# Kernel optimization log

Hardware: AMD Instinct MI355X
Metric: run time of the kernel (lower is better)

Reference implementation:

```python
import jax, jax.numpy as jnp
import numpy as np
from jax import lax

D = 768          # embed_dim
H = 12           # n_heads
DEPTH = 2
T = 6            # n_timepoints
PS = 7           # patch_size
IMG = (56, 49, 49)
GRID = (8, 7, 7)
NPATCH = 392     # prod(GRID), must be even for the sinusoidal PE
SEQ = T * NPATCH # 2352 space-time tokens
MLP_H = 3072     # int(768 * 4.0)
B = 2
RRELU_MLP = 0.4        # eval-mode RReLU(0.1, 0.7) slope
RRELU_HEAD = 11.0/48.0 # eval-mode RReLU(1/8, 1/3) slope


def _ln(x, g, b, eps=1e-6):
    m = x.mean(-1, keepdims=True)
    v = ((x - m) ** 2).mean(-1, keepdims=True)
    return (x - m) / jnp.sqrt(v + eps) * g + b


def _pos_enc(t, d):
    pos = np.arange(t, dtype=np.float32)[:, None]
    div = 1.0 / 10000.0 ** (np.arange(0, d, 2, dtype=np.float32) / d)
    pe = np.zeros((t, d), np.float32)
    pe[:, 0::2] = np.sin(pos * div)
    pe[:, 1::2] = np.cos(pos * div)
    return jnp.asarray(pe)


def _convT_dw(x, w, bias, stride, dilation):
    # depthwise ConvTranspose3d(C, C, k, stride, dilation, groups=C); w: (C,1,k,k,k)
    C = x.shape[1]
    k = w.shape[-1]
    wf = jnp.flip(w, axis=(2, 3, 4))
    pad = (k - 1) * dilation
    y = lax.conv_general_dilated(
        x, wf, window_strides=(1, 1, 1), padding=[(pad, pad)] * 3,
        lhs_dilation=(stride,) * 3, rhs_dilation=(dilation,) * 3,
        dimension_numbers=('NCDHW', 'OIDHW', 'NCDHW'), feature_group_count=C)
    return y + bias[None, :, None, None, None]


def _nearest(x, size):
    # torch F.interpolate(mode='nearest'): src = floor(dst * in/out)
    for ax, s in zip((2, 3, 4), size):
        idx = (jnp.arange(s) * (x.shape[ax] / s)).astype(jnp.int32)
        x = jnp.take(x, idx, axis=ax)
    return x


def setup_inputs() -> dict:
    key = jax.random.key(0)
    ks = iter(jax.random.split(key, 64))
    def rn(shape, s=0.02):
        return jax.random.normal(next(ks), shape, jnp.float32) * s
    inp = {}
    inp['x'] = jax.random.normal(next(ks), (B, 1, T) + IMG, jnp.float32)
    inp['pconv_w'] = rn((D, 1, PS, PS, PS)); inp['pconv_b'] = rn((D,))
    inp['pos_embed'] = rn((1, SEQ, D))
    inp['ln1_g'] = jnp.ones((DEPTH, D)); inp['ln1_b'] = jnp.zeros((DEPTH, D))
    inp['qkv_w'] = rn((DEPTH, 3 * D, D)); inp['qkv_b'] = rn((DEPTH, 3 * D))
    inp['proj_w'] = rn((DEPTH, D, D)); inp['proj_b'] = rn((DEPTH, D))
    inp['ln2_g'] = jnp.ones((DEPTH, D)); inp['ln2_b'] = jnp.zeros((DEPTH, D))
    inp['fc1_w'] = rn((DEPTH, MLP_H, D)); inp['fc1_b'] = rn((DEPTH, MLP_H))
    inp['fc2_w'] = rn((DEPTH, D, MLP_H)); inp['fc2_b'] = rn((DEPTH, D))
    inp['normf_g'] = jnp.ones((D,)); inp['normf_b'] = jnp.zeros((D,))
    inp['dfc_w'] = rn((1, D)); inp['dfc_b'] = rn((1,))
    inp['up1_w'] = rn((T, 1, 7, 7, 7)); inp['up1_b'] = rn((T,))
    inp['up2_w'] = rn((T, 1, 5, 5, 5)); inp['up2_b'] = rn((T,))
    inp['up3_w'] = rn((T, 1, 9, 9, 9)); inp['up3_b'] = rn((T,))
    inp['hconv_w'] = rn((T, 1, 1, 1, 1)); inp['hconv_b'] = rn((T,))
    return inp


def reference(x, pconv_w, pconv_b, pos_embed, ln1_g, ln1_b, qkv_w, qkv_b,
              proj_w, proj_b, ln2_g, ln2_b, fc1_w, fc1_b, fc2_w, fc2_b,
              normf_g, normf_b, dfc_w, dfc_b, up1_w, up1_b, up2_w, up2_b,
              up3_w, up3_b, hconv_w, hconv_b):
    b = x.shape[0]
    hd = D // H
    scale = hd ** -0.5
    # fold time into batch, patch-embed each 3D frame
    xt = x.transpose(0, 2, 1, 3, 4, 5).reshape(b * T, 1, *IMG)
    y = lax.conv_general_dilated(
        xt, pconv_w, (PS, PS, PS), 'VALID',
        dimension_numbers=('NCDHW', 'OIDHW', 'NCDHW'))
    y = y + pconv_b[None, :, None, None, None]
    tok = y.reshape(b * T, D, NPATCH).transpose(0, 2, 1).reshape(b, SEQ, D)
    tok = tok + pos_embed
    for i in range(DEPTH):
        h = _ln(tok, ln1_g[i], ln1_b[i])
        qkv = (h @ qkv_w[i].T + qkv_b[i]).reshape(b, SEQ, 3, H, hd)
        qkv = qkv.transpose(2, 0, 3, 1, 4)  # (3,b,H,SEQ,hd)
        q, k, v = qkv[0], qkv[1], qkv[2]
        attn = jax.nn.softmax(jnp.einsum('bhnd,bhmd->bhnm', q, k) * scale, axis=-1)
        o = jnp.einsum('bhnm,bhmd->bhnd', attn, v)
        o = o.transpose(0, 2, 1, 3).reshape(b, SEQ, D)
        tok = tok + (o @ proj_w[i].T + proj_b[i])
        h = _ln(tok, ln2_g[i], ln2_b[i])
        h = h @ fc1_w[i].T + fc1_b[i]
        h = jnp.where(h >= 0, h, RRELU_MLP * h)
        tok = tok + (h @ fc2_w[i].T + fc2_b[i])
    tok = _ln(tok, normf_g, normf_b)
    z = tok.reshape(b, T, NPATCH, D)
    # --- DecoderHead ---
    z = (z @ dfc_w.T + dfc_b)[..., 0]           # (b,T,NPATCH)
    z = z - z.mean(axis=1, keepdims=True)       # subtract time mean
    z = z + _pos_enc(T, NPATCH)
    z = z.reshape(b, T, *GRID)                  # (b,T,8,7,7)
    z = _convT_dw(z, up1_w, up1_b, 1, 1)        # -> (b,T,14,13,13)
    z = _convT_dw(z, up2_w, up2_b, 2, 1)        # -> (b,T,31,29,29)
    z = _convT_dw(z, up3_w, up3_b, 1, 2)        # -> (b,T,47,45,45)
    z = _nearest(z, IMG)                        # -> (b,T,56,49,49)
    z = z * hconv_w[:, 0, 0, 0, 0][None, :, None, None, None] \
        + hconv_b[None, :, None, None, None]
    z = jnp.where(z >= 0, z, RRELU_HEAD * z)
    return z[:, None].transpose(0, 1, 3, 4, 5, 2)  # (b,1,56,49,49,T)
```

## Files before the change

kernel.cpp:

```cpp
#include <hip/hip_runtime.h>


#define AS1 __attribute__((address_space(1)))
#define AS3 __attribute__((address_space(3)))

using bf16 = __bf16;
typedef __bf16 bf16x8 __attribute__((ext_vector_type(8)));
typedef float  f32x4  __attribute__((ext_vector_type(4)));

#define CDIV(a, b) (((a) + (b) - 1) / (b))

__device__ __forceinline__ void gll16(const void* g, void* l) {
  __builtin_amdgcn_global_load_lds((AS1 void*)(void*)g, (AS3 void*)l, 16, 0, 0);
}

template <int SH>
__device__ __forceinline__ float rorf(float x) {
  int i = __builtin_amdgcn_update_dpp(0, __builtin_bit_cast(int, x),
                                      0x120 + SH, 0xF, 0xF, false);
  return __builtin_bit_cast(float, i);
}
__device__ __forceinline__ float rowmax16(float v) {
  v = fmaxf(v, rorf<1>(v)); v = fmaxf(v, rorf<2>(v));
  v = fmaxf(v, rorf<4>(v)); v = fmaxf(v, rorf<8>(v));
  return v;
}
__device__ __forceinline__ float rowsum16(float v) {
  v += rorf<1>(v); v += rorf<2>(v); v += rorf<4>(v); v += rorf<8>(v);
  return v;
}

__global__ __launch_bounds__(256) void gemm_bt(
    const bf16* __restrict__ A, const bf16* __restrict__ B,
    float* Cf, bf16* Cb, const float* __restrict__ bias,
    const float* addp, int addmod, int rrelu,
    int M, int N, int K, int lda, int ldb, int ldc,
    long long sA, long long sB, long long sC, int ksplit) {
  __shared__ __align__(16) bf16 As[128 * 32];
  __shared__ __align__(16) bf16 Bs[128 * 32];
  const int tid  = threadIdx.x;
  const int lane = tid & 63;
  const int wave = tid >> 6;
  const int wm = wave & 1;
  const int wn = wave >> 1;
  const int q  = lane >> 4;
  const int r  = lane & 15;
  const int tm0 = blockIdx.x * 128;
  const int tn0 = blockIdx.y * 128;
  const int z   = blockIdx.z;

  const bf16* Ab = A + (ksplit > 1 ? 0 : (size_t)z * (size_t)sA);
  const bf16* Bb = B + (ksplit > 1 ? 0 : (size_t)z * (size_t)sB);
  const int kc = K / ksplit;
  const int kb = (ksplit > 1) ? z * kc : 0;
  const int ke = (ksplit > 1) ? kb + kc : K;

  const int arow0 = min(tm0 + (tid >> 2), M - 1);
  const int arow1 = min(tm0 + (tid >> 2) + 64, M - 1);
  const int brow0 = min(tn0 + (tid >> 2), N - 1);
  const int brow1 = min(tn0 + (tid >> 2) + 64, N - 1);
  const int kcol  = (tid & 3) * 8;
  const bf16* ap0 = Ab + (size_t)arow0 * lda + kcol;
  const bf16* ap1 = Ab + (size_t)arow1 * lda + kcol;
  const bf16* bp0 = Bb + (size_t)brow0 * ldb + kcol;
  const bf16* bp1 = Bb + (size_t)brow1 * ldb + kcol;
  bf16* asw0 = &As[(wave * 64) * 8];
  bf16* asw1 = &As[(256 + wave * 64) * 8];
  bf16* bsw0 = &Bs[(wave * 64) * 8];
  bf16* bsw1 = &Bs[(256 + wave * 64) * 8];

  f32x4 acc[4][4];
#pragma unroll
  for (int mi = 0; mi < 4; ++mi)
#pragma unroll
    for (int ni = 0; ni < 4; ++ni) acc[mi][ni] = (f32x4){0.f, 0.f, 0.f, 0.f};

  for (int k0 = kb; k0 < ke; k0 += 32) {
    __syncthreads();
    gll16(ap0 + k0, asw0);
    gll16(ap1 + k0, asw1);
    gll16(bp0 + k0, bsw0);
    gll16(bp1 + k0, bsw1);
    __syncthreads();
    bf16x8 af[4], bfr[4];
#pragma unroll
    for (int mi = 0; mi < 4; ++mi)
      af[mi] = *(const bf16x8*)&As[(wm * 64 + mi * 16 + r) * 32 + q * 8];
#pragma unroll
    for (int ni = 0; ni < 4; ++ni)
      bfr[ni] = *(const bf16x8*)&Bs[(wn * 64 + ni * 16 + r) * 32 + q * 8];
#pragma unroll
    for (int mi = 0; mi < 4; ++mi)
#pragma unroll
      for (int ni = 0; ni < 4; ++ni)
        acc[mi][ni] = __builtin_amdgcn_mfma_f32_16x16x32_bf16(
            af[mi], bfr[ni], acc[mi][ni], 0, 0, 0);
  }

  float* cf = Cf ? Cf + (ksplit > 1 ? 0 : (size_t)z * (size_t)sC) : nullptr;
  bf16*  cb = Cb ? Cb + (ksplit > 1 ? 0 : (size_t)z * (size_t)sC) : nullptr;
#pragma unroll
  for (int mi = 0; mi < 4; ++mi) {
    const int row0 = tm0 + wm * 64 + mi * 16 + q * 4;
#pragma unroll
    for (int ni = 0; ni < 4; ++ni) {
      const int col = tn0 + wn * 64 + ni * 16 + r;
      if (col >= N) continue;
      const float bv = bias ? bias[col] : 0.f;
#pragma unroll
      for (int reg = 0; reg < 4; ++reg) {
        const int rr = row0 + reg;
        if (rr >= M) continue;
        if (ksplit > 1) {
          float v = acc[mi][ni][reg] + (z == 0 ? bv : 0.f);
          atomicAdd(&cf[(size_t)rr * ldc + col], v);
        } else {
          float v = acc[mi][ni][reg] + bv;
          if (addp) v += addp[(size_t)(rr % addmod) * ldc + col];
          if (rrelu) v = (v >= 0.f) ? v : 0.4f * v;
          if (cf) cf[(size_t)rr * ldc + col] = v;
          else    cb[(size_t)rr * ldc + col] = (bf16)v;
        }
      }
    }
  }
}

__global__ __launch_bounds__(256) void flash_attn_split(
    const bf16* __restrict__ Qg, const bf16* __restrict__ Kg,
    const bf16* __restrict__ Vt, float* __restrict__ Opart,
    float* __restrict__ Mpart, float* __restrict__ Lpart) {
  __shared__ __align__(16) bf16 Plds[4][2][16 * 72];
  const int lane = threadIdx.x & 63;
  const int wave = threadIdx.x >> 6;
  const int q = lane >> 4, r = lane & 15;
  const int inst = blockIdx.y;
  const int z = blockIdx.z;
  const int rt = blockIdx.x * 4 + wave;
  if (rt >= 74) return;
  const int row0 = rt * 32;
  const int ch0 = (z * 37) >> 1;
  const int ch1 = ((z + 1) * 37) >> 1;
  const bf16* Qi = Qg + (size_t)inst * 2432 * 64;
  const bf16* Ki = Kg + (size_t)inst * 2368 * 64;
  const bf16* Vi = Vt + (size_t)inst * 64 * 2368;

  bf16x8 qf[2][2];
#pragma unroll
  for (int t = 0; t < 2; ++t) {
    qf[t][0] = *(const bf16x8*)&Qi[(size_t)(row0 + t * 16 + r) * 64 + q * 8];
    qf[t][1] = *(const bf16x8*)&Qi[(size_t)(row0 + t * 16 + r) * 64 + 32 + q * 8];
  }

  f32x4 O[2][4];
  float m[2][4], l[2][4];
#pragma unroll
  for (int t = 0; t < 2; ++t)
#pragma unroll
    for (int i = 0; i < 4; ++i) {
      O[t][i] = (f32x4){0.f, 0.f, 0.f, 0.f};
      m[t][i] = -1e30f; l[t][i] = 0.f;
    }

  bf16x8 kf0[4], kf1[4];
#pragma unroll
  for (int ct = 0; ct < 4; ++ct) {
    const bf16* kp = &Ki[(size_t)(ch0 * 64 + ct * 16 + r) * 64 + q * 8];
    kf0[ct] = *(const bf16x8*)kp;
    kf1[ct] = *(const bf16x8*)(kp + 32);
  }

  for (int ch = ch0; ch < ch1; ++ch) {
    const int col0 = ch * 64;
    bf16x8 vf0[4], vf1[4];
#pragma unroll
    for (int ot = 0; ot < 4; ++ot) {
      const bf16* vp = &Vi[(size_t)(ot * 16 + r) * 2368 + col0 + q * 8];
      vf0[ot] = *(const bf16x8*)vp;
      vf1[ot] = *(const bf16x8*)(vp + 32);
    }
    f32x4 s[2][4];
#pragma unroll
    for (int ct = 0; ct < 4; ++ct) {
#pragma unroll
      for (int t = 0; t < 2; ++t) {
        f32x4 a = (f32x4){0.f, 0.f, 0.f, 0.f};
        a = __builtin_amdgcn_mfma_f32_16x16x32_bf16(qf[t][0], kf0[ct], a, 0, 0, 0);
        a = __builtin_amdgcn_mfma_f32_16x16x32_bf16(qf[t][1], kf1[ct], a, 0, 0, 0);
        s[t][ct] = a * 0.125f;
      }
    }
    if (ch == 36) {
      s[0][3] = (f32x4){-1e30f, -1e30f, -1e30f, -1e30f};
      s[1][3] = (f32x4){-1e30f, -1e30f, -1e30f, -1e30f};
    }
    const int chn = (ch + 1 < 37) ? ch + 1 : 36;
#pragma unroll
    for (int ct = 0; ct < 4; ++ct) {
      const bf16* kp = &Ki[(size_t)(chn * 64 + ct * 16 + r) * 64 + q * 8];
      kf0[ct] = *(const bf16x8*)kp;
      kf1[ct] = *(const bf16x8*)(kp + 32);
    }
#pragma unroll
    for (int t = 0; t < 2; ++t) {
      float alpha[4];
#pragma unroll
      for (int reg = 0; reg < 4; ++reg) {
        float v = fmaxf(fmaxf(s[t][0][reg], s[t][1][reg]),
                        fmaxf(s[t][2][reg], s[t][3][reg]));
        v = rowmax16(v);
        float nm = fmaxf(m[t][reg], v);
        alpha[reg] = __expf(m[t][reg] - nm);
        m[t][reg] = nm;
      }
      float csum[4] = {0.f, 0.f, 0.f, 0.f};
#pragma unroll
      for (int ct = 0; ct < 4; ++ct)
#pragma unroll
        for (int reg = 0; reg < 4; ++reg) {
          float p = __expf(s[t][ct][reg] - m[t][reg]);
          s[t][ct][reg] = p;
          csum[reg] += p;
        }
#pragma unroll
      for (int reg = 0; reg < 4; ++reg)
        l[t][reg] = l[t][reg] * alpha[reg] + rowsum16(csum[reg]);
#pragma unroll
      for (int ot = 0; ot < 4; ++ot)
#pragma unroll
        for (int reg = 0; reg < 4; ++reg) O[t][ot][reg] *= alpha[reg];
      bf16* Pw = Plds[wave][t];
#pragma unroll
      for (int ct = 0; ct < 4; ++ct)
#pragma unroll
        for (int reg = 0; reg < 4; ++reg)
          Pw[(q * 4 + reg) * 72 + ct * 16 + r] = (bf16)s[t][ct][reg];
    }
#pragma unroll
    for (int t = 0; t < 2; ++t) {
      const bf16* Pw = Plds[wave][t];
      const bf16x8 pf0 = *(const bf16x8*)&Pw[r * 72 + q * 8];
      const bf16x8 pf1 = *(const bf16x8*)&Pw[r * 72 + 32 + q * 8];
#pragma unroll
      for (int ot = 0; ot < 4; ++ot) {
        O[t][ot] = __builtin_amdgcn_mfma_f32_16x16x32_bf16(pf0, vf0[ot], O[t][ot], 0, 0, 0);
        O[t][ot] = __builtin_amdgcn_mfma_f32_16x16x32_bf16(pf1, vf1[ot], O[t][ot], 0, 0, 0);
      }
    }
  }
#pragma unroll
  for (int t = 0; t < 2; ++t) {
    const int p = (z * 24 + inst) * 152 + rt * 2 + t;
    float* Op = Opart + (size_t)p * 1024;
#pragma unroll
    for (int ot = 0; ot < 4; ++ot)
#pragma unroll
      for (int reg = 0; reg < 4; ++reg)
        Op[(q * 4 + reg) * 64 + ot * 16 + r] = O[t][ot][reg];
    if (r == 0) {
#pragma unroll
      for (int reg = 0; reg < 4; ++reg) {
        Mpart[(size_t)p * 16 + q * 4 + reg] = m[t][reg];
        Lpart[(size_t)p * 16 + q * 4 + reg] = l[t][reg];
      }
    }
  }
}

__global__ __launch_bounds__(256) void attn_combine(
    const float* __restrict__ Opart, const float* __restrict__ Mpart,
    const float* __restrict__ Lpart, bf16* __restrict__ Og) {
  const int tile = blockIdx.x;
  const int inst = blockIdx.y;
  const int bb = inst / 12, hh = inst % 12;
  const int pb = inst * 152 + tile;
#pragma unroll
  for (int i = 0; i < 4; ++i) {
    const int e = threadIdx.x + 256 * i;
    const int row = e >> 6, col = e & 63;
    float mv[2], lv[2];
#pragma unroll
    for (int zz = 0; zz < 2; ++zz) {
      mv[zz] = Mpart[(size_t)(zz * 3648 + pb) * 16 + row];
      lv[zz] = Lpart[(size_t)(zz * 3648 + pb) * 16 + row];
    }
    const float ms = fmaxf(mv[0], mv[1]);
    float lsum = 0.f, osum = 0.f;
#pragma unroll
    for (int zz = 0; zz < 2; ++zz) {
      const float w = __expf(mv[zz] - ms);
      lsum += lv[zz] * w;
      osum += Opart[(size_t)(zz * 3648 + pb) * 1024 + e] * w;
    }
    Og[(size_t)(bb * 2352 + tile * 16 + row) * 768 + hh * 64 + col] =
        (bf16)(osum / lsum);
  }
}


__global__ void cvt_bf16(const float* __restrict__ x, bf16* __restrict__ y, int n) {
  int i = blockIdx.x * 256 + threadIdx.x;
  if (i < n) y[i] = (bf16)x[i];
}

__global__ void prep_pconv(const float* __restrict__ w, bf16* __restrict__ y) {
  int i = blockIdx.x * 256 + threadIdx.x;
  if (i >= 768 * 352) return;
  int d = i / 352, j = i % 352;
  y[i] = (bf16)(j < 343 ? w[d * 343 + j] : 0.f);
}

__global__ void im2col(const float* __restrict__ x, bf16* __restrict__ A) {
  int i = blockIdx.x * 256 + threadIdx.x;
  if (i >= 4704 * 352) return;
  int j = i % 352, tok = i / 352;
  float v = 0.f;
  if (j < 343) {
    int p = tok % 392, bt = tok / 392;
    int kx = j % 7, ky = (j / 7) % 7, kz = j / 49;
    int px = p % 7, py = (p / 7) % 7, pz = p / 49;
    int zz = pz * 7 + kz, yy = py * 7 + ky, xx = px * 7 + kx;
    v = x[(((size_t)bt * 56 + zz) * 49 + yy) * 49 + xx];
  }
  A[i] = (bf16)v;
}

template <typename OT>
__global__ __launch_bounds__(256) void ln_kernel(
    const float* __restrict__ x, const float* __restrict__ g,
    const float* __restrict__ bb, OT* __restrict__ y, int M) {
  int row = blockIdx.x * 4 + (threadIdx.x >> 6);
  int lane = threadIdx.x & 63;
  if (row >= M) return;
  const float* xr = x + (size_t)row * 768;
  float v[12], s = 0.f;
#pragma unroll
  for (int i = 0; i < 12; ++i) { v[i] = xr[lane + i * 64]; s += v[i]; }
#pragma unroll
  for (int off = 32; off; off >>= 1) s += __shfl_xor(s, off, 64);
  float mean = s * (1.f / 768.f);
  float vs = 0.f;
#pragma unroll
  for (int i = 0; i < 12; ++i) { float d = v[i] - mean; vs += d * d; }
#pragma unroll
  for (int off = 32; off; off >>= 1) vs += __shfl_xor(vs, off, 64);
  float inv = 1.f / sqrtf(vs * (1.f / 768.f) + 1e-6f);
#pragma unroll
  for (int i = 0; i < 12; ++i) {
    int j = lane + i * 64;
    y[(size_t)row * 768 + j] = (OT)((v[i] - mean) * inv * g[j] + bb[j]);
  }
}

__global__ __launch_bounds__(256) void repack_qkv(
    const float* __restrict__ qkv, bf16* __restrict__ Q,
    bf16* __restrict__ Kb, bf16* __restrict__ VT) {
  int inst = blockIdx.y;
  int b = inst / 12, h = inst % 12;
  int s = blockIdx.x * 4 + (threadIdx.x >> 6);
  int d = threadIdx.x & 63;
  if (s >= 2432) return;
  size_t qIdx = ((size_t)inst * 2432 + s) * 64 + d;
  if (s >= 2352) {
    Q[qIdx] = (bf16)0.f;
    if (s < 2368) {
      Kb[((size_t)inst * 2368 + s) * 64 + d] = (bf16)0.f;
      VT[((size_t)inst * 64 + d) * 2368 + s] = (bf16)0.f;
    }
    return;
  }
  const float* rowp = qkv + (size_t)(b * 2352 + s) * 2304 + h * 64 + d;
  Q[qIdx] = (bf16)rowp[0];
  Kb[((size_t)inst * 2368 + s) * 64 + d] = (bf16)rowp[768];
  VT[((size_t)inst * 64 + d) * 2368 + s] = (bf16)rowp[1536];
}

__global__ __launch_bounds__(256) void dfc_kernel(
    const float* __restrict__ x, const float* __restrict__ w,
    const float* __restrict__ b0, float* __restrict__ z0, int M) {
  int row = blockIdx.x * 4 + (threadIdx.x >> 6);
  int lane = threadIdx.x & 63;
  if (row >= M) return;
  const float* xr = x + (size_t)row * 768;
  float s = 0.f;
#pragma unroll
  for (int i = 0; i < 12; ++i) s += xr[lane + i * 64] * w[lane + i * 64];
#pragma unroll
  for (int off = 32; off; off >>= 1) s += __shfl_xor(s, off, 64);
  if (lane == 0) z0[row] = s + b0[0];
}

__global__ void head_pe(const float* __restrict__ z0, float* __restrict__ z1) {
  int i = blockIdx.x * 256 + threadIdx.x;
  if (i >= 784) return;
  int b = i / 392, p = i % 392;
  float vals[6], m = 0.f;
#pragma unroll
  for (int t = 0; t < 6; ++t) { vals[t] = z0[(b * 6 + t) * 392 + p]; m += vals[t]; }
  m *= (1.f / 6.f);
  float e = (float)(2 * (p >> 1)) / 392.0f;
  float div = powf(10000.f, -e);
#pragma unroll
  for (int t = 0; t < 6; ++t) {
    float arg = (float)t * div;
    float pe = (p & 1) ? cosf(arg) : sinf(arg);
    z1[(b * 6 + t) * 392 + p] = vals[t] - m + pe;
  }
}

template <int ID, int IH, int IW, int PD, int PH, int PWA, int OFF, int ST>
__global__ void pad_in(const float* __restrict__ x, float* __restrict__ Xp) {
  int i = blockIdx.x * 256 + threadIdx.x;
  constexpr int total = 12 * PD * PH * PWA;
  if (i >= total) return;
  int px = i % PWA, t1 = i / PWA;
  int py = t1 % PH, t2 = t1 / PH;
  int pz = t2 % PD, c = t2 / PD;
  float v = 0.f;
  int tz = pz - OFF, ty = py - OFF, tx = px - OFF;
  if (tz >= 0 && ty >= 0 && tx >= 0 &&
      (ST == 1 || (((tz | ty | tx) & 1) == 0))) {
    int iz = tz / ST, iy = ty / ST, ix = tx / ST;
    if (iz < ID && iy < IH && ix < IW)
      v = x[((size_t)(c * ID + iz) * IH + iy) * IW + ix];
  }
  Xp[i] = v;
}

template <int PD, int PH, int PWA, int OD, int OH, int OW, int K, int DIL>
__global__ __launch_bounds__(256) void convt4(
    const float* __restrict__ Xp, const float* __restrict__ w,
    const float* __restrict__ bias, float* __restrict__ y) {
  constexpr int P0  = (K - 1) * DIL;
  constexpr int QX  = (OW + 3) / 4;
  constexpr int NLD = (P0 + 4 + 3) / 4;
  int idx = blockIdx.x * 256 + threadIdx.x;
  if (idx >= OD * OH * QX) return;
  int c = blockIdx.y;
  int qx = idx % QX; int t1 = idx / QX;
  int oy = t1 % OH;  int oz = t1 / OH;
  int ox0 = qx * 4;
  const float* xc = Xp + (size_t)c * (PD * PH * PWA);
  const float* wc = w + (c % 6) * (K * K * K);
  const float bv = bias[c % 6];
  float a0 = bv, a1 = bv, a2 = bv, a3 = bv;
  for (int kz = 0; kz < K; ++kz) {
    const int bz = oz + P0 - kz * DIL;
#pragma unroll
    for (int ky = 0; ky < K; ++ky) {
      const int by = oy + P0 - ky * DIL;
      const float* base = xc + ((size_t)bz * PH + by) * PWA + ox0;
      float buf[NLD * 4];
#pragma unroll
      for (int i = 0; i < NLD; ++i)
        *(f32x4*)&buf[i * 4] = *(const f32x4*)(base + i * 4);
      const float* wr = wc + (kz * K + ky) * K;
#pragma unroll
      for (int kx = 0; kx < K; ++kx) {
        const float wv = wr[kx];
        const int j = P0 - kx * DIL;
        a0 += wv * buf[j + 0];
        a1 += wv * buf[j + 1];
        a2 += wv * buf[j + 2];
        a3 += wv * buf[j + 3];
      }
    }
  }
  float* yp = y + (size_t)c * (OD * OH * OW) + ((size_t)oz * OH + oy) * OW + ox0;
  yp[0] = a0;
  if (ox0 + 1 < OW) yp[1] = a1;
  if (ox0 + 2 < OW) yp[2] = a2;
  if (ox0 + 3 < OW) yp[3] = a3;
}

__global__ void head_final(const float* __restrict__ z4, const float* __restrict__ hw,
                           const float* __restrict__ hb, float* __restrict__ out) {
  int idx = blockIdx.x * 256 + threadIdx.x;
  if (idx >= 1613472) return;
  int t = idx % 6, rdx = idx / 6;
  int xx = rdx % 49; rdx /= 49;
  int yy = rdx % 49; rdx /= 49;
  int zz = rdx % 56; int b = rdx / 56;
  const float rz = (float)(47.0 / 56.0), ry = (float)(45.0 / 49.0);
  int iz = (int)((float)zz * rz);
  int iy = (int)((float)yy * ry);
  int ix = (int)((float)xx * ry);
  float v = z4[(((size_t)(b * 6 + t) * 47 + iz) * 45 + iy) * 45 + ix];
  v = v * hw[t] + hb[t];
  v = (v >= 0.f) ? v : (11.0f / 48.0f) * v;
  out[idx] = v;
}


static inline void launch_gemm(hipStream_t s, const bf16* A, const bf16* B,
                               float* Cf, bf16* Cb, const float* bias,
                               const float* addp, int addmod, int rrelu,
                               int M, int N, int K, int lda, int ldb, int ldc,
                               long long sA, long long sB, long long sC,
                               int nz, int ksplit = 1) {
  dim3 g(CDIV(M, 128), CDIV(N, 128), ksplit > 1 ? ksplit : nz);
  gemm_bt<<<g, 256, 0, s>>>(A, B, Cf, Cb, bias, addp, addmod, rrelu,
                            M, N, K, lda, ldb, ldc, sA, sB, sC, ksplit);
}

extern "C" void kernel_launch(void* const* d_in, const int* in_sizes, int n_in,
                              void* d_out, int out_size, void* d_ws, size_t ws_size,
                              hipStream_t stream) {
  (void)in_sizes; (void)n_in; (void)out_size; (void)ws_size;
  const float* x       = (const float*)d_in[0];
  const float* pconv_w = (const float*)d_in[1];
  const float* pconv_b = (const float*)d_in[2];
  const float* pos_emb = (const float*)d_in[3];
  const float* ln1_g   = (const float*)d_in[4];
  const float* ln1_b   = (const float*)d_in[5];
  const float* qkv_wf  = (const float*)d_in[6];
  const float* qkv_b   = (const float*)d_in[7];
  const float* proj_wf = (const float*)d_in[8];
  const float* proj_b  = (const float*)d_in[9];
  const float* ln2_g   = (const float*)d_in[10];
  const float* ln2_b   = (const float*)d_in[11];
  const float* fc1_wf  = (const float*)d_in[12];
  const float* fc1_b   = (const float*)d_in[13];
  const float* fc2_wf  = (const float*)d_in[14];
  const float* fc2_b   = (const float*)d_in[15];
  const float* normf_g = (const float*)d_in[16];
  const float* normf_b = (const float*)d_in[17];
  const float* dfc_w   = (const float*)d_in[18];
  const float* dfc_b   = (const float*)d_in[19];
  const float* up1_w   = (const float*)d_in[20];
  const float* up1_b   = (const float*)d_in[21];
  const float* up2_w   = (const float*)d_in[22];
  const float* up2_b   = (const float*)d_in[23];
  const float* up3_w   = (const float*)d_in[24];
  const float* up3_b   = (const float*)d_in[25];
  const float* hconv_w = (const float*)d_in[26];
  const float* hconv_b = (const float*)d_in[27];
  float* out = (float*)d_out;

  char* ws = (char*)d_ws;
  size_t off = 0;
  auto alloc = [&](size_t bytes) -> void* {
    void* p = ws + off;
    off += (bytes + 255) & ~(size_t)255;
    return p;
  };
  float* tok   = (float*)alloc(4704UL * 768 * 4);
  bf16* lnout  = (bf16*)alloc(4704UL * 768 * 2);
  float* qkv   = (float*)alloc(4704UL * 2304 * 4);
  bf16* Qb     = (bf16*)alloc(24UL * 2432 * 64 * 2);
  bf16* Kb     = (bf16*)alloc(24UL * 2368 * 64 * 2);
  bf16* VT     = (bf16*)alloc(24UL * 64 * 2368 * 2);
  bf16* attnb  = (bf16*)alloc(4704UL * 768 * 2);
  bf16* hb     = (bf16*)alloc(4704UL * 3072 * 2);
  bf16* Apatch = (bf16*)alloc(4704UL * 352 * 2);
  bf16* Wq     = (bf16*)alloc(2UL * 2304 * 768 * 2);
  bf16* Wp     = (bf16*)alloc(2UL * 768 * 768 * 2);
  bf16* W1     = (bf16*)alloc(2UL * 3072 * 768 * 2);
  bf16* W2     = (bf16*)alloc(2UL * 768 * 3072 * 2);
  bf16* Wpc    = (bf16*)alloc(768UL * 352 * 2);
  float* Opart = (float*)alloc(2UL * 24 * 152 * 1024 * 4);
  float* Mpart = (float*)alloc(2UL * 24 * 152 * 16 * 4);
  float* Lpart = (float*)alloc(2UL * 24 * 152 * 16 * 4);
  float* z0    = (float*)alloc(4704UL * 4);
  float* z1    = (float*)alloc(4704UL * 4);
  float* z2    = (float*)alloc(12UL * 14 * 13 * 13 * 4);
  float* z3    = (float*)alloc(12UL * 31 * 29 * 29 * 4);
  float* z4    = (float*)alloc(12UL * 47 * 45 * 45 * 4);
  float* p1    = (float*)alloc(12UL * 20 * 19 * 24 * 4);
  float* p2    = (float*)alloc(12UL * 35 * 33 * 36 * 4);
  float* p3    = (float*)alloc(12UL * 63 * 61 * 64 * 4);
  float* lnf   = qkv;

  cvt_bf16<<<CDIV(3538944, 256), 256, 0, stream>>>(qkv_wf, Wq, 3538944);
  cvt_bf16<<<CDIV(1179648, 256), 256, 0, stream>>>(proj_wf, Wp, 1179648);
  cvt_bf16<<<CDIV(4718592, 256), 256, 0, stream>>>(fc1_wf, W1, 4718592);
  cvt_bf16<<<CDIV(4718592, 256), 256, 0, stream>>>(fc2_wf, W2, 4718592);
  prep_pconv<<<CDIV(768 * 352, 256), 256, 0, stream>>>(pconv_w, Wpc);

  im2col<<<CDIV(4704 * 352, 256), 256, 0, stream>>>(x, Apatch);
  launch_gemm(stream, Apatch, Wpc, tok, nullptr, pconv_b, pos_emb, 2352, 0,
              4704, 768, 352, 352, 352, 768, 0, 0, 0, 1);

  for (int i = 0; i < 2; ++i) {
    ln_kernel<bf16><<<1176, 256, 0, stream>>>(tok, ln1_g + i * 768, ln1_b + i * 768, lnout, 4704);
    launch_gemm(stream, lnout, Wq + (size_t)i * 2304 * 768, qkv, nullptr,
                qkv_b + i * 2304, nullptr, 1, 0,
                4704, 2304, 768, 768, 768, 2304, 0, 0, 0, 1);
    repack_qkv<<<dim3(608, 24), 256, 0, stream>>>(qkv, Qb, Kb, VT);
    flash_attn_split<<<dim3(19, 24, 2), 256, 0, stream>>>(Qb, Kb, VT, Opart, Mpart, Lpart);
    attn_combine<<<dim3(147, 24), 256, 0, stream>>>(Opart, Mpart, Lpart, attnb);
    launch_gemm(stream, attnb, Wp + (size_t)i * 768 * 768, tok, nullptr,
                proj_b + i * 768, nullptr, 1, 0,
                4704, 768, 768, 768, 768, 768, 0, 0, 0, 1, 4);
    ln_kernel<bf16><<<1176, 256, 0, stream>>>(tok, ln2_g + i * 768, ln2_b + i * 768, lnout, 4704);
    launch_gemm(stream, lnout, W1 + (size_t)i * 3072 * 768, nullptr, hb,
                fc1_b + i * 3072, nullptr, 1, 1,
                4704, 3072, 768, 768, 768, 3072, 0, 0, 0, 1);
    launch_gemm(stream, hb, W2 + (size_t)i * 768 * 3072, tok, nullptr,
                fc2_b + i * 768, nullptr, 1, 0,
                4704, 768, 3072, 3072, 3072, 768, 0, 0, 0, 1, 4);
  }

  ln_kernel<float><<<1176, 256, 0, stream>>>(tok, normf_g, normf_b, lnf, 4704);
  dfc_kernel<<<1176, 256, 0, stream>>>(lnf, dfc_w, dfc_b, z0, 4704);
  head_pe<<<4, 256, 0, stream>>>(z0, z1);

  pad_in<8, 7, 7, 20, 19, 24, 6, 1>
      <<<CDIV(12 * 20 * 19 * 24, 256), 256, 0, stream>>>(z1, p1);
  convt4<20, 19, 24, 14, 13, 13, 7, 1>
      <<<dim3(CDIV(14 * 13 * 4, 256), 12), 256, 0, stream>>>(p1, up1_w, up1_b, z2);
  pad_in<14, 13, 13, 35, 33, 36, 4, 2>
      <<<CDIV(12 * 35 * 33 * 36, 256), 256, 0, stream>>>(z2, p2);
  convt4<35, 33, 36, 31, 29, 29, 5, 1>
      <<<dim3(CDIV(31 * 29 * 8, 256), 12), 256, 0, stream>>>(p2, up2_w, up2_b, z3);
  pad_in<31, 29, 29, 63, 61, 64, 16, 1>
      <<<CDIV(12 * 63 * 61 * 64, 256), 256, 0, stream>>>(z3, p3);
  convt4<63, 61, 64, 47, 45, 45, 9, 2>
      <<<dim3(CDIV(47 * 45 * 12, 256), 12), 256, 0, stream>>>(p3, up3_w, up3_b, z4);

  head_final<<<CDIV(1613472, 256), 256, 0, stream>>>(z4, hconv_w, hconv_b, out);
}
```

Before: 1.201 ms.

## Split attention KV into three chunks, split-K patch and QKV GEMMs, use exp2

```diff
diff --git a/kernel.cpp b/kernel.cpp
--- a/kernel.cpp
+++ b/kernel.cpp
@@ -51,9 +51,12 @@
 
   const bf16* Ab = A + (ksplit > 1 ? 0 : (size_t)z * (size_t)sA);
   const bf16* Bb = B + (ksplit > 1 ? 0 : (size_t)z * (size_t)sB);
-  const int kc = K / ksplit;
-  const int kb = (ksplit > 1) ? z * kc : 0;
-  const int ke = (ksplit > 1) ? kb + kc : K;
+  int kb = 0, ke = K;
+  if (ksplit > 1) {
+    const int kc = ((K / ksplit + 31) / 32) * 32;
+    kb = z * kc;
+    ke = min(kb + kc, K);
+  }
 
   const int arow0 = min(tm0 + (tid >> 2), M - 1);
   const int arow1 = min(tm0 + (tid >> 2) + 64, M - 1);
@@ -112,7 +115,11 @@
         const int rr = row0 + reg;
         if (rr >= M) continue;
         if (ksplit > 1) {
-          float v = acc[mi][ni][reg] + (z == 0 ? bv : 0.f);
+          float v = acc[mi][ni][reg];
+          if (z == 0) {
+            v += bv;
+            if (addp) v += addp[(size_t)(rr % addmod) * ldc + col];
+          }
           atomicAdd(&cf[(size_t)rr * ldc + col], v);
         } else {
           float v = acc[mi][ni][reg] + bv;
@@ -139,8 +146,8 @@
   const int rt = blockIdx.x * 4 + wave;
   if (rt >= 74) return;
   const int row0 = rt * 32;
-  const int ch0 = (z * 37) >> 1;
-  const int ch1 = ((z + 1) * 37) >> 1;
+  const int ch0 = (z * 37) / 3;
+  const int ch1 = ((z + 1) * 37) / 3;
   const bf16* Qi = Qg + (size_t)inst * 2432 * 64;
   const bf16* Ki = Kg + (size_t)inst * 2368 * 64;
   const bf16* Vi = Vt + (size_t)inst * 64 * 2368;
@@ -187,7 +194,7 @@
         f32x4 a = (f32x4){0.f, 0.f, 0.f, 0.f};
         a = __builtin_amdgcn_mfma_f32_16x16x32_bf16(qf[t][0], kf0[ct], a, 0, 0, 0);
         a = __builtin_amdgcn_mfma_f32_16x16x32_bf16(qf[t][1], kf1[ct], a, 0, 0, 0);
-        s[t][ct] = a * 0.125f;
+        s[t][ct] = a;
       }
     }
     if (ch == 36) {
@@ -210,7 +217,7 @@
                         fmaxf(s[t][2][reg], s[t][3][reg]));
         v = rowmax16(v);
         float nm = fmaxf(m[t][reg], v);
-        alpha[reg] = __expf(m[t][reg] - nm);
+        alpha[reg] = exp2f(m[t][reg] - nm);
         m[t][reg] = nm;
       }
       float csum[4] = {0.f, 0.f, 0.f, 0.f};
@@ -218,7 +225,7 @@
       for (int ct = 0; ct < 4; ++ct)
 #pragma unroll
         for (int reg = 0; reg < 4; ++reg) {
-          float p = __expf(s[t][ct][reg] - m[t][reg]);
+          float p = exp2f(s[t][ct][reg] - m[t][reg]);
           s[t][ct][reg] = p;
           csum[reg] += p;
         }
@@ -278,17 +285,17 @@
   for (int i = 0; i < 4; ++i) {
     const int e = threadIdx.x + 256 * i;
     const int row = e >> 6, col = e & 63;
-    float mv[2], lv[2];
-#pragma unroll
-    for (int zz = 0; zz < 2; ++zz) {
+    float mv[3], lv[3];
+#pragma unroll
+    for (int zz = 0; zz < 3; ++zz) {
       mv[zz] = Mpart[(size_t)(zz * 3648 + pb) * 16 + row];
       lv[zz] = Lpart[(size_t)(zz * 3648 + pb) * 16 + row];
     }
-    const float ms = fmaxf(mv[0], mv[1]);
+    const float ms = fmaxf(fmaxf(mv[0], mv[1]), mv[2]);
     float lsum = 0.f, osum = 0.f;
 #pragma unroll
-    for (int zz = 0; zz < 2; ++zz) {
-      const float w = __expf(mv[zz] - ms);
+    for (int zz = 0; zz < 3; ++zz) {
+      const float w = exp2f(mv[zz] - ms);
       lsum += lv[zz] * w;
       osum += Opart[(size_t)(zz * 3648 + pb) * 1024 + e] * w;
     }
@@ -297,6 +304,11 @@
   }
 }
 
+
+__global__ void zero_f32(float* __restrict__ p, int n4) {
+  int i = blockIdx.x * 256 + threadIdx.x;
+  if (i < n4) ((f32x4*)p)[i] = (f32x4){0.f, 0.f, 0.f, 0.f};
+}
 
 __global__ void cvt_bf16(const float* __restrict__ x, bf16* __restrict__ y, int n) {
   int i = blockIdx.x * 256 + threadIdx.x;
@@ -371,7 +383,7 @@
   }
   const float* rowp = qkv + (size_t)(b * 2352 + s) * 2304 + h * 64 + d;
   Q[qIdx] = (bf16)rowp[0];
-  Kb[((size_t)inst * 2368 + s) * 64 + d] = (bf16)rowp[768];
+  Kb[((size_t)inst * 2368 + s) * 64 + d] = (bf16)(rowp[768] * 0.18033688f);
   VT[((size_t)inst * 64 + d) * 2368 + s] = (bf16)rowp[1536];
 }
 
@@ -558,9 +570,9 @@
   bf16* W1     = (bf16*)alloc(2UL * 3072 * 768 * 2);
   bf16* W2     = (bf16*)alloc(2UL * 768 * 3072 * 2);
   bf16* Wpc    = (bf16*)alloc(768UL * 352 * 2);
-  float* Opart = (float*)alloc(2UL * 24 * 152 * 1024 * 4);
-  float* Mpart = (float*)alloc(2UL * 24 * 152 * 16 * 4);
-  float* Lpart = (float*)alloc(2UL * 24 * 152 * 16 * 4);
+  float* Opart = (float*)alloc(3UL * 24 * 152 * 1024 * 4);
+  float* Mpart = (float*)alloc(3UL * 24 * 152 * 16 * 4);
+  float* Lpart = (float*)alloc(3UL * 24 * 152 * 16 * 4);
   float* z0    = (float*)alloc(4704UL * 4);
   float* z1    = (float*)alloc(4704UL * 4);
   float* z2    = (float*)alloc(12UL * 14 * 13 * 13 * 4);
@@ -569,7 +581,7 @@
   float* p1    = (float*)alloc(12UL * 20 * 19 * 24 * 4);
   float* p2    = (float*)alloc(12UL * 35 * 33 * 36 * 4);
   float* p3    = (float*)alloc(12UL * 63 * 61 * 64 * 4);
-  float* lnf   = qkv;
+  float* lnf   = (float*)alloc(4704UL * 768 * 4);
 
   cvt_bf16<<<CDIV(3538944, 256), 256, 0, stream>>>(qkv_wf, Wq, 3538944);
   cvt_bf16<<<CDIV(1179648, 256), 256, 0, stream>>>(proj_wf, Wp, 1179648);
@@ -578,16 +590,18 @@
   prep_pconv<<<CDIV(768 * 352, 256), 256, 0, stream>>>(pconv_w, Wpc);
 
   im2col<<<CDIV(4704 * 352, 256), 256, 0, stream>>>(x, Apatch);
+  zero_f32<<<CDIV(4704 * 768 / 4, 256), 256, 0, stream>>>(tok, 4704 * 768 / 4);
   launch_gemm(stream, Apatch, Wpc, tok, nullptr, pconv_b, pos_emb, 2352, 0,
-              4704, 768, 352, 352, 352, 768, 0, 0, 0, 1);
+              4704, 768, 352, 352, 352, 768, 0, 0, 0, 1, 2);
 
   for (int i = 0; i < 2; ++i) {
     ln_kernel<bf16><<<1176, 256, 0, stream>>>(tok, ln1_g + i * 768, ln1_b + i * 768, lnout, 4704);
+    zero_f32<<<CDIV(4704 * 2304 / 4, 256), 256, 0, stream>>>(qkv, 4704 * 2304 / 4);
     launch_gemm(stream, lnout, Wq + (size_t)i * 2304 * 768, qkv, nullptr,
                 qkv_b + i * 2304, nullptr, 1, 0,
-                4704, 2304, 768, 768, 768, 2304, 0, 0, 0, 1);
+                4704, 2304, 768, 768, 768, 2304, 0, 0, 0, 1, 2);
     repack_qkv<<<dim3(608, 24), 256, 0, stream>>>(qkv, Qb, Kb, VT);
-    flash_attn_split<<<dim3(19, 24, 2), 256, 0, stream>>>(Qb, Kb, VT, Opart, Mpart, Lpart);
+    flash_attn_split<<<dim3(19, 24, 3), 256, 0, stream>>>(Qb, Kb, VT, Opart, Mpart, Lpart);
     attn_combine<<<dim3(147, 24), 256, 0, stream>>>(Opart, Mpart, Lpart, attnb);
     launch_gemm(stream, attnb, Wp + (size_t)i * 768 * 768, tok, nullptr,
                 proj_b + i * 768, nullptr, 1, 0,
```

Measured after the change: 1.352 ms. 12.6% more time.

## Fuse QKV repack into GEMM epilogue and fold softmax scale into K

Applied to the files above, without the earlier changes.

```diff
diff --git a/kernel.cpp b/kernel.cpp
--- a/kernel.cpp
+++ b/kernel.cpp
@@ -35,7 +35,8 @@
     float* Cf, bf16* Cb, const float* __restrict__ bias,
     const float* addp, int addmod, int rrelu,
     int M, int N, int K, int lda, int ldb, int ldc,
-    long long sA, long long sB, long long sC, int ksplit) {
+    long long sA, long long sB, long long sC, int ksplit,
+    bf16* __restrict__ Qo, bf16* __restrict__ Ko, bf16* __restrict__ Vo) {
   __shared__ __align__(16) bf16 As[128 * 32];
   __shared__ __align__(16) bf16 Bs[128 * 32];
   const int tid  = threadIdx.x;
@@ -51,9 +52,12 @@
 
   const bf16* Ab = A + (ksplit > 1 ? 0 : (size_t)z * (size_t)sA);
   const bf16* Bb = B + (ksplit > 1 ? 0 : (size_t)z * (size_t)sB);
-  const int kc = K / ksplit;
-  const int kb = (ksplit > 1) ? z * kc : 0;
-  const int ke = (ksplit > 1) ? kb + kc : K;
+  int kb = 0, ke = K;
+  if (ksplit > 1) {
+    const int kc = ((K / ksplit + 31) / 32) * 32;
+    kb = z * kc;
+    ke = min(kb + kc, K);
+  }
 
   const int arow0 = min(tm0 + (tid >> 2), M - 1);
   const int arow1 = min(tm0 + (tid >> 2) + 64, M - 1);
@@ -111,8 +115,26 @@
       for (int reg = 0; reg < 4; ++reg) {
         const int rr = row0 + reg;
         if (rr >= M) continue;
-        if (ksplit > 1) {
-          float v = acc[mi][ni][reg] + (z == 0 ? bv : 0.f);
+        if (Qo) {
+          const float v = acc[mi][ni][reg] + bv;
+          const int which = col / 768;
+          const int hh = (col % 768) >> 6;
+          const int dd = col & 63;
+          const int bb2 = rr / 2352;
+          const int ss = rr - bb2 * 2352;
+          const int inst = bb2 * 12 + hh;
+          if (which == 0)
+            Qo[((size_t)inst * 2432 + ss) * 64 + dd] = (bf16)v;
+          else if (which == 1)
+            Ko[((size_t)inst * 2368 + ss) * 64 + dd] = (bf16)(v * 0.18033688f);
+          else
+            Vo[((size_t)inst * 64 + dd) * 2368 + ss] = (bf16)v;
+        } else if (ksplit > 1) {
+          float v = acc[mi][ni][reg];
+          if (z == 0) {
+            v += bv;
+            if (addp) v += addp[(size_t)(rr % addmod) * ldc + col];
+          }
           atomicAdd(&cf[(size_t)rr * ldc + col], v);
         } else {
           float v = acc[mi][ni][reg] + bv;
@@ -187,7 +209,7 @@
         f32x4 a = (f32x4){0.f, 0.f, 0.f, 0.f};
         a = __builtin_amdgcn_mfma_f32_16x16x32_bf16(qf[t][0], kf0[ct], a, 0, 0, 0);
         a = __builtin_amdgcn_mfma_f32_16x16x32_bf16(qf[t][1], kf1[ct], a, 0, 0, 0);
-        s[t][ct] = a * 0.125f;
+        s[t][ct] = a;
       }
     }
     if (ch == 36) {
@@ -210,7 +232,7 @@
                         fmaxf(s[t][2][reg], s[t][3][reg]));
         v = rowmax16(v);
         float nm = fmaxf(m[t][reg], v);
-        alpha[reg] = __expf(m[t][reg] - nm);
+        alpha[reg] = exp2f(m[t][reg] - nm);
         m[t][reg] = nm;
       }
       float csum[4] = {0.f, 0.f, 0.f, 0.f};
@@ -218,7 +240,7 @@
       for (int ct = 0; ct < 4; ++ct)
 #pragma unroll
         for (int reg = 0; reg < 4; ++reg) {
-          float p = __expf(s[t][ct][reg] - m[t][reg]);
+          float p = exp2f(s[t][ct][reg] - m[t][reg]);
           s[t][ct][reg] = p;
           csum[reg] += p;
         }
@@ -288,7 +310,7 @@
     float lsum = 0.f, osum = 0.f;
 #pragma unroll
     for (int zz = 0; zz < 2; ++zz) {
-      const float w = __expf(mv[zz] - ms);
+      const float w = exp2f(mv[zz] - ms);
       lsum += lv[zz] * w;
       osum += Opart[(size_t)(zz * 3648 + pb) * 1024 + e] * w;
     }
@@ -297,6 +319,23 @@
   }
 }
 
+
+__global__ void zero_pads(bf16* __restrict__ Q, bf16* __restrict__ Kb,
+                          bf16* __restrict__ VT) {
+  int i = blockIdx.x * 256 + threadIdx.x;
+  if (i < 122880) {
+    int inst = i / 5120, rem = i % 5120;
+    Q[((size_t)inst * 2432 + 2352 + rem / 64) * 64 + (rem & 63)] = (bf16)0.f;
+  }
+  if (i < 24576) {
+    int inst = i / 1024, rem = i % 1024;
+    Kb[((size_t)inst * 2368 + 2352 + rem / 64) * 64 + (rem & 63)] = (bf16)0.f;
+  }
+  if (i < 24576) {
+    int inst = i / 1024, rem = i % 1024;
+    VT[((size_t)inst * 64 + rem / 16) * 2368 + 2352 + (rem & 15)] = (bf16)0.f;
+  }
+}
 
 __global__ void cvt_bf16(const float* __restrict__ x, bf16* __restrict__ y, int n) {
   int i = blockIdx.x * 256 + threadIdx.x;
@@ -350,29 +389,6 @@
     int j = lane + i * 64;
     y[(size_t)row * 768 + j] = (OT)((v[i] - mean) * inv * g[j] + bb[j]);
   }
-}
-
-__global__ __launch_bounds__(256) void repack_qkv(
-    const float* __restrict__ qkv, bf16* __restrict__ Q,
-    bf16* __restrict__ Kb, bf16* __restrict__ VT) {
-  int inst = blockIdx.y;
-  int b = inst / 12, h = inst % 12;
-  int s = blockIdx.x * 4 + (threadIdx.x >> 6);
-  int d = threadIdx.x & 63;
-  if (s >= 2432) return;
-  size_t qIdx = ((size_t)inst * 2432 + s) * 64 + d;
-  if (s >= 2352) {
-    Q[qIdx] = (bf16)0.f;
-    if (s < 2368) {
-      Kb[((size_t)inst * 2368 + s) * 64 + d] = (bf16)0.f;
-      VT[((size_t)inst * 64 + d) * 2368 + s] = (bf16)0.f;
-    }
-    return;
-  }
-  const float* rowp = qkv + (size_t)(b * 2352 + s) * 2304 + h * 64 + d;
-  Q[qIdx] = (bf16)rowp[0];
-  Kb[((size_t)inst * 2368 + s) * 64 + d] = (bf16)rowp[768];
-  VT[((size_t)inst * 64 + d) * 2368 + s] = (bf16)rowp[1536];
 }
 
 __global__ __launch_bounds__(256) void dfc_kernel(
@@ -497,10 +513,13 @@
                                const float* addp, int addmod, int rrelu,
                                int M, int N, int K, int lda, int ldb, int ldc,
                                long long sA, long long sB, long long sC,
-                               int nz, int ksplit = 1) {
+                               int nz, int ksplit = 1,
+                               bf16* Qo = nullptr, bf16* Ko = nullptr,
+                               bf16* Vo = nullptr) {
   dim3 g(CDIV(M, 128), CDIV(N, 128), ksplit > 1 ? ksplit : nz);
   gemm_bt<<<g, 256, 0, s>>>(A, B, Cf, Cb, bias, addp, addmod, rrelu,
-                            M, N, K, lda, ldb, ldc, sA, sB, sC, ksplit);
+                            M, N, K, lda, ldb, ldc, sA, sB, sC, ksplit,
+                            Qo, Ko, Vo);
 }
 
 extern "C" void kernel_launch(void* const* d_in, const int* in_sizes, int n_in,
@@ -546,7 +565,6 @@
   };
   float* tok   = (float*)alloc(4704UL * 768 * 4);
   bf16* lnout  = (bf16*)alloc(4704UL * 768 * 2);
-  float* qkv   = (float*)alloc(4704UL * 2304 * 4);
   bf16* Qb     = (bf16*)alloc(24UL * 2432 * 64 * 2);
   bf16* Kb     = (bf16*)alloc(24UL * 2368 * 64 * 2);
   bf16* VT     = (bf16*)alloc(24UL * 64 * 2368 * 2);
@@ -569,13 +587,14 @@
   float* p1    = (float*)alloc(12UL * 20 * 19 * 24 * 4);
   float* p2    = (float*)alloc(12UL * 35 * 33 * 36 * 4);
   float* p3    = (float*)alloc(12UL * 63 * 61 * 64 * 4);
-  float* lnf   = qkv;
+  float* lnf   = (float*)alloc(4704UL * 768 * 4);
 
   cvt_bf16<<<CDIV(3538944, 256), 256, 0, stream>>>(qkv_wf, Wq, 3538944);
   cvt_bf16<<<CDIV(1179648, 256), 256, 0, stream>>>(proj_wf, Wp, 1179648);
   cvt_bf16<<<CDIV(4718592, 256), 256, 0, stream>>>(fc1_wf, W1, 4718592);
   cvt_bf16<<<CDIV(4718592, 256), 256, 0, stream>>>(fc2_wf, W2, 4718592);
   prep_pconv<<<CDIV(768 * 352, 256), 256, 0, stream>>>(pconv_w, Wpc);
+  zero_pads<<<CDIV(122880, 256), 256, 0, stream>>>(Qb, Kb, VT);
 
   im2col<<<CDIV(4704 * 352, 256), 256, 0, stream>>>(x, Apatch);
   launch_gemm(stream, Apatch, Wpc, tok, nullptr, pconv_b, pos_emb, 2352, 0,
@@ -583,10 +602,9 @@
 
   for (int i = 0; i < 2; ++i) {
     ln_kernel<bf16><<<1176, 256, 0, stream>>>(tok, ln1_g + i * 768, ln1_b + i * 768, lnout, 4704);
-    launch_gemm(stream, lnout, Wq + (size_t)i * 2304 * 768, qkv, nullptr,
+    launch_gemm(stream, lnout, Wq + (size_t)i * 2304 * 768, nullptr, nullptr,
                 qkv_b + i * 2304, nullptr, 1, 0,
-                4704, 2304, 768, 768, 768, 2304, 0, 0, 0, 1);
-    repack_qkv<<<dim3(608, 24), 256, 0, stream>>>(qkv, Qb, Kb, VT);
+                4704, 2304, 768, 768, 768, 2304, 0, 0, 0, 1, 1, Qb, Kb, VT);
     flash_attn_split<<<dim3(19, 24, 2), 256, 0, stream>>>(Qb, Kb, VT, Opart, Mpart, Lpart);
     attn_combine<<<dim3(147, 24), 256, 0, stream>>>(Opart, Mpart, Lpart, attnb);
     launch_gemm(stream, attnb, Wp + (size_t)i * 768 * 768, tok, nullptr,
```

After: 1.175 ms. 1.02x faster.
